# Performance work log

Measured on AMD Instinct MI355X. Metric: run time of the kernel, lower is better.

Reference implementation:

```python
import math
import jax, jax.numpy as jnp
import numpy as np

D_MODEL = 1024
NUM_HEADS = 16
HEAD_DIM = D_MODEL // NUM_HEADS
MAX_REL = 128


def setup_inputs() -> dict:
    key = jax.random.key(0)
    ks = jax.random.split(key, 7)
    B, S = 2, 2048
    s = 1.0 / math.sqrt(D_MODEL)
    return {
        "x": jax.random.normal(ks[0], (B, S, D_MODEL), dtype=jnp.float32),
        "mask": jnp.ones((B, S, S), dtype=jnp.int32),
        "w_q": jax.random.normal(ks[1], (D_MODEL, D_MODEL), dtype=jnp.float32) * s,
        "w_k": jax.random.normal(ks[2], (D_MODEL, D_MODEL), dtype=jnp.float32) * s,
        "w_v": jax.random.normal(ks[3], (D_MODEL, D_MODEL), dtype=jnp.float32) * s,
        "w_o_w": jax.random.normal(ks[4], (D_MODEL, D_MODEL), dtype=jnp.float32) * s,
        "w_o_b": jnp.zeros((D_MODEL,), dtype=jnp.float32),
        "rel_emb": jax.random.normal(ks[5], (2 * MAX_REL + 1, HEAD_DIM), dtype=jnp.float32),
    }


def reference(x, mask, w_q, w_k, w_v, w_o_w, w_o_b, rel_emb):
    B, S, D = x.shape
    H, hd = NUM_HEADS, HEAD_DIM
    scale = math.sqrt(hd)

    def proj(w):  # torch Linear: x @ w.T  -> [B,H,S,hd]
        return (x @ w.T).reshape(B, S, H, hd).transpose(0, 2, 1, 3)

    Q, K, V = proj(w_q), proj(w_k), proj(w_v)

    # content scores (scaled)
    scores = jnp.einsum("bhqd,bhkd->bhqk", Q, K) / scale

    # T5-style relative position bias (NOT scaled, matching source)
    pos = jnp.arange(S)
    dist = jnp.clip(pos[None, :] - pos[:, None], -MAX_REL, MAX_REL) + MAX_REL  # [S,S]
    rel = rel_emb[dist]  # [S,S,hd]
    scores = scores + jnp.einsum("bhqd,qkd->bhqk", Q, rel)

    scores = jnp.where(mask[:, None, :, :] == 0, -1e9, scores)
    attn = jax.nn.softmax(scores, axis=-1)  # [B,H,S,S]

    ctx = jnp.einsum("bhqk,bhkd->bhqd", attn, V)
    ctx = ctx.transpose(0, 2, 1, 3).reshape(B, S, D)
    out = ctx @ w_o_w.T + w_o_b
    return out, attn
```

## Files before the change

### kernel.cpp

```cpp
#include <hip/hip_runtime.h>
#include <hip/hip_bf16.h>

#define B_ 2
#define S_ 2048
#define H_ 16
#define HD_ 64
#define D_ 1024
#define NJ_ 257
#define RSTRIDE_ 264

typedef __bf16 v8bf __attribute__((ext_vector_type(8)));
typedef __bf16 v4bf __attribute__((ext_vector_type(4)));
typedef float  v4f  __attribute__((ext_vector_type(4)));

static __device__ __forceinline__ v4f mfma16(v8bf a, v8bf b, v4f c) {
    return __builtin_amdgcn_mfma_f32_16x16x32_bf16(a, b, c, 0, 0, 0);
}

__global__ void k_split2(const float* __restrict__ src, __bf16* __restrict__ h,
                         __bf16* __restrict__ l, int n4) {
    int i = blockIdx.x * blockDim.x + threadIdx.x;
    int stride = gridDim.x * blockDim.x;
    for (; i < n4; i += stride) {
        const float4 v = ((const float4*)src)[i];
        float vv[4] = {v.x, v.y, v.z, v.w};
        v4bf hv, lv;
#pragma unroll
        for (int j = 0; j < 4; j++) {
            __bf16 hb = (__bf16)vv[j];
            hv[j] = hb;
            lv[j] = (__bf16)(vv[j] - (float)hb);
        }
        *(v4bf*)(h + 4 * (size_t)i) = hv;
        *(v4bf*)(l + 4 * (size_t)i) = lv;
    }
}

__global__ void k_cast4(const float* __restrict__ w0, const float* __restrict__ w1,
                        const float* __restrict__ w2, const float* __restrict__ w3,
                        __bf16* __restrict__ o0, __bf16* __restrict__ o1,
                        __bf16* __restrict__ o2, __bf16* __restrict__ o3) {
    const int n4each = (D_ * D_) / 4;
    int i = blockIdx.x * blockDim.x + threadIdx.x;
    int stride = gridDim.x * blockDim.x;
    for (; i < 4 * n4each; i += stride) {
        const int region = i >> 18, j = i & (n4each - 1);
        const float* src = region == 0 ? w0 : region == 1 ? w1 : region == 2 ? w2 : w3;
        __bf16* dst = region == 0 ? o0 : region == 1 ? o1 : region == 2 ? o2 : o3;
        const float4 v = ((const float4*)src)[j];
        v4bf o = {(__bf16)v.x, (__bf16)v.y, (__bf16)v.z, (__bf16)v.w};
        *(v4bf*)(dst + 4 * (size_t)j) = o;
    }
}

__global__ void k_rowflag(const int* __restrict__ mask, unsigned char* __restrict__ flags) {
    const int row = blockIdx.x;
    const int4* mp = (const int4*)(mask + (size_t)row * S_);
    int ok = 1;
    for (int i = threadIdx.x; i < S_ / 4; i += blockDim.x) {
        int4 m = mp[i];
        ok &= (m.x != 0) & (m.y != 0) & (m.z != 0) & (m.w != 0);
    }
    int all = __syncthreads_and(ok);
    if (threadIdx.x == 0) flags[row] = (unsigned char)(all != 0);
}

__global__ __launch_bounds__(256) void k_projQKV(const __bf16* __restrict__ xh,
                                                 const __bf16* __restrict__ xl,
                                                 const __bf16* __restrict__ wqh,
                                                 const __bf16* __restrict__ wkh,
                                                 const __bf16* __restrict__ wvh,
                                                 __bf16* __restrict__ Qh,
                                                 __bf16* __restrict__ Ql,
                                                 __bf16* __restrict__ Kh,
                                                 __bf16* __restrict__ Vb) {
    __shared__ __bf16 sXh[64][72], sXl[64][72], sW[64][72];
    const int seg = blockIdx.x >> 4;
    const int n0 = (blockIdx.x & 15) * 64;
    const int m0 = blockIdx.y * 64;
    const __bf16* W = seg == 0 ? wqh : (seg == 1 ? wkh : wvh);
    const int tid = threadIdx.x, lane = tid & 63, wid = tid >> 6;
    const int fr = lane & 15, fo = (lane >> 4) * 8;
    const int srow = tid >> 2, scol = (tid & 3) * 16;
    v4f acc[4] = {};
    for (int k0 = 0; k0 < D_; k0 += 64) {
        const size_t ga = (size_t)(m0 + srow) * D_ + k0 + scol;
        const size_t gb = (size_t)(n0 + srow) * D_ + k0 + scol;
        *(v8bf*)&sXh[srow][scol]     = *(const v8bf*)(xh + ga);
        *(v8bf*)&sXh[srow][scol + 8] = *(const v8bf*)(xh + ga + 8);
        if (seg < 2) {
            *(v8bf*)&sXl[srow][scol]     = *(const v8bf*)(xl + ga);
            *(v8bf*)&sXl[srow][scol + 8] = *(const v8bf*)(xl + ga + 8);
        }
        *(v8bf*)&sW[srow][scol]     = *(const v8bf*)(W + gb);
        *(v8bf*)&sW[srow][scol + 8] = *(const v8bf*)(W + gb + 8);
        __syncthreads();
#pragma unroll
        for (int ks = 0; ks < 2; ks++) {
            v8bf ah = *(const v8bf*)&sXh[wid * 16 + fr][ks * 32 + fo];
            v8bf al;
            if (seg < 2) al = *(const v8bf*)&sXl[wid * 16 + fr][ks * 32 + fo];
#pragma unroll
            for (int nt = 0; nt < 4; nt++) {
                v8bf bb = *(const v8bf*)&sW[nt * 16 + fr][ks * 32 + fo];
                acc[nt] = mfma16(ah, bb, acc[nt]);
                if (seg < 2) acc[nt] = mfma16(al, bb, acc[nt]);
            }
        }
        __syncthreads();
    }
#pragma unroll
    for (int nt = 0; nt < 4; nt++) {
#pragma unroll
        for (int r = 0; r < 4; r++) {
            const int row = m0 + wid * 16 + (lane >> 4) * 4 + r;
            const int col = n0 + nt * 16 + fr;
            const size_t idx = (size_t)row * D_ + col;
            const float f = acc[nt][r];
            if (seg == 0) {
                __bf16 hb = (__bf16)f;
                Qh[idx] = hb;
                Ql[idx] = (__bf16)(f - (float)hb);
            } else if (seg == 1) {
                Kh[idx] = (__bf16)f;
            } else {
                Vb[idx] = (__bf16)f;
            }
        }
    }
}

__global__ __launch_bounds__(256) void k_vtrans(const __bf16* __restrict__ Vb,
                                                __bf16* __restrict__ Vt) {
    __shared__ __bf16 t[64][72];
    const int s0 = blockIdx.x * 64, n0 = blockIdx.y * 64, b = blockIdx.z;
    const int tid = threadIdx.x;
    const int r = tid >> 2, c = (tid & 3) * 16;
    const size_t gin = ((size_t)(b * S_ + s0 + r)) * D_ + n0 + c;
    *(v8bf*)&t[r][c]     = *(const v8bf*)(Vb + gin);
    *(v8bf*)&t[r][c + 8] = *(const v8bf*)(Vb + gin + 8);
    __syncthreads();
    v8bf o0, o1;
#pragma unroll
    for (int j = 0; j < 8; j++) { o0[j] = t[c + j][r]; o1[j] = t[c + 8 + j][r]; }
    const size_t gout = ((size_t)(b * D_ + n0 + r)) * S_ + s0 + c;
    *(v8bf*)(Vt + gout)     = o0;
    *(v8bf*)(Vt + gout + 8) = o1;
}

__global__ __launch_bounds__(256) void k_relgemm(const __bf16* __restrict__ Qh,
                                                 const __bf16* __restrict__ Ql,
                                                 const __bf16* __restrict__ relh,
                                                 const __bf16* __restrict__ rell,
                                                 float* __restrict__ Rg,
                                                 float* __restrict__ qnorm,
                                                 float* __restrict__ Rmax) {
    const int q0 = blockIdx.x * 64;
    const int bh = blockIdx.y;
    const int b = bh >> 4, h = bh & 15;
    const int tid = threadIdx.x, lane = tid & 63, wid = tid >> 6;
    const int fr = lane & 15, fo = (lane >> 4) * 8;
    const size_t qbase = (size_t)(b * S_ + q0 + wid * 16 + fr) * D_ + h * HD_;
    v8bf qa_h[2], qa_l[2];
#pragma unroll
    for (int ks = 0; ks < 2; ks++) {
        qa_h[ks] = *(const v8bf*)(Qh + qbase + ks * 32 + fo);
        qa_l[ks] = *(const v8bf*)(Ql + qbase + ks * 32 + fo);
    }

    float qs = 0.0f;
#pragma unroll
    for (int ks = 0; ks < 2; ks++)
#pragma unroll
        for (int j = 0; j < 8; j++) {
            const float v = (float)qa_h[ks][j] + (float)qa_l[ks][j];
            qs += v * v;
        }
    qs += __shfl_xor(qs, 16);
    qs += __shfl_xor(qs, 32);
    if ((lane >> 4) == 0) qnorm[(size_t)bh * S_ + q0 + wid * 16 + fr] = sqrtf(qs);

    v4f acc[17] = {};
#pragma unroll
    for (int jt = 0; jt < 17; jt++) {
        int j = jt * 16 + fr;
        if (j > 256) j = 256;
        const size_t rb = (size_t)j * HD_;
#pragma unroll
        for (int ks = 0; ks < 2; ks++) {
            v8bf bh_ = *(const v8bf*)(relh + rb + ks * 32 + fo);
            v8bf bl_ = *(const v8bf*)(rell + rb + ks * 32 + fo);
            acc[jt] = mfma16(qa_h[ks], bh_, acc[jt]);
            acc[jt] = mfma16(qa_h[ks], bl_, acc[jt]);
            acc[jt] = mfma16(qa_l[ks], bh_, acc[jt]);
        }
    }

    float rm[4] = {-3.0e38f, -3.0e38f, -3.0e38f, -3.0e38f};
#pragma unroll
    for (int jt = 0; jt < 17; jt++)
#pragma unroll
        for (int r = 0; r < 4; r++) rm[r] = fmaxf(rm[r], acc[jt][r]);
#pragma unroll
    for (int r = 0; r < 4; r++) {
#pragma unroll
        for (int sh = 1; sh < 16; sh <<= 1) rm[r] = fmaxf(rm[r], __shfl_xor(rm[r], sh));
    }
    if (fr == 0) {
#pragma unroll
        for (int r = 0; r < 4; r++)
            Rmax[(size_t)bh * S_ + q0 + wid * 16 + (lane >> 4) * 4 + r] = rm[r];
    }

    const size_t rowbase = ((size_t)bh * S_ + q0 + wid * 16 + (lane >> 4) * 4) * RSTRIDE_;
#pragma unroll
    for (int jt = 0; jt < 17; jt++) {
        const int j = jt * 16 + fr;
        if (j <= 256) {
#pragma unroll
            for (int r = 0; r < 4; r++)
                Rg[rowbase + (size_t)r * RSTRIDE_ + j] = acc[jt][r];
        }
    }
}

__global__ __launch_bounds__(256) void k_knorm(const __bf16* __restrict__ Kh,
                                               float* __restrict__ Kmax) {
    __shared__ float red[4];
    const int bh = blockIdx.x, b = bh >> 4, h = bh & 15;
    const int tid = threadIdx.x;
    float best = 0.0f;
#pragma unroll
    for (int i = 0; i < 8; i++) {
        const int k = tid + i * 256;
        const __bf16* kr = Kh + (size_t)(b * S_ + k) * D_ + h * HD_;
        float s = 0.0f;
#pragma unroll
        for (int j = 0; j < 8; j++) {
            v8bf v = *(const v8bf*)(kr + j * 8);
#pragma unroll
            for (int e = 0; e < 8; e++) { const float f = (float)v[e]; s += f * f; }
        }
        best = fmaxf(best, s);
    }
#pragma unroll
    for (int sh = 1; sh < 64; sh <<= 1) best = fmaxf(best, __shfl_xor(best, sh));
    if ((tid & 63) == 0) red[tid >> 6] = best;
    __syncthreads();
    if (tid == 0)
        Kmax[bh] = sqrtf(fmaxf(fmaxf(red[0], red[1]), fmaxf(red[2], red[3])));
}

__global__ __launch_bounds__(512, 4) void k_attnE(const __bf16* __restrict__ Qh,
                                                  const __bf16* __restrict__ Ql,
                                                  const __bf16* __restrict__ Kh,
                                                  const __bf16* __restrict__ Vt,
                                                  const float* __restrict__ Rg,
                                                  const int* __restrict__ mask,
                                                  const unsigned char* __restrict__ flags,
                                                  const float* __restrict__ qnorm,
                                                  const float* __restrict__ Rmax,
                                                  const float* __restrict__ Kmax,
                                                  __bf16* __restrict__ E,
                                                  float* __restrict__ lrowInv,
                                                  __bf16* __restrict__ ctx) {
    __shared__ __bf16 sK[2][64][72], sV[2][64][72], sP[128][72];
    const int flat = blockIdx.x;
    const int swz = (flat & 7) * 64 + (flat >> 3);
    const int qt = swz & 15, bh = swz >> 4;
    const int b = bh >> 4, h = bh & 15;
    const int q0 = qt * 128;
    const int tid = threadIdx.x, lane = tid & 63, w = tid >> 6;
    const int fr = lane & 15, fq = lane >> 4, fo = fq * 8;
    const int myrow = w * 16 + fq * 4;
    const int srow = tid >> 3, sc8 = (tid & 7) * 8;

    const size_t qbase = (size_t)(b * S_ + q0 + w * 16 + fr) * D_ + h * HD_;
    v8bf qa_h[2], qa_l[2];
#pragma unroll
    for (int ks = 0; ks < 2; ks++) {
        qa_h[ks] = *(const v8bf*)(Qh + qbase + ks * 32 + fo);
        qa_l[ks] = *(const v8bf*)(Ql + qbase + ks * 32 + fo);
    }

    const int qg0 = q0 + myrow;
    const size_t rbase0 = ((size_t)bh * S_ + qg0) * RSTRIDE_;
    const size_t mbase0 = ((size_t)b * S_ + qg0) * S_;
    float rcL[4], rcR[4], mhat[4];
    int flr[4];
    const float km = Kmax[bh] * 0.125f;
#pragma unroll
    for (int r = 0; r < 4; r++) {
        rcL[r] = Rg[rbase0 + (size_t)r * RSTRIDE_];
        rcR[r] = Rg[rbase0 + (size_t)r * RSTRIDE_ + 256];
        flr[r] = flags[(size_t)b * S_ + qg0 + r];
        mhat[r] = Rmax[(size_t)bh * S_ + qg0 + r] +
                  qnorm[(size_t)bh * S_ + qg0 + r] * km + 0.5f;
    }

    const __bf16* kgbase = Kh + (size_t)(b * S_ + srow) * D_ + h * HD_ + sc8;
    const __bf16* vgbase = Vt + (size_t)(b * D_ + h * HD_ + srow) * S_ + sc8;
    v8bf rk = *(const v8bf*)(kgbase);
    v8bf rv = *(const v8bf*)(vgbase);
    *(v8bf*)&sK[0][srow][sc8] = rk;
    *(v8bf*)&sV[0][srow][sc8] = rv;
    rk = *(const v8bf*)(kgbase + (size_t)64 * D_);
    rv = *(const v8bf*)(vgbase + 64);
    __syncthreads();

    float lrun[4] = {0.0f, 0.0f, 0.0f, 0.0f};
    v4f acc2[4] = {};
    int cur = 0;
    for (int kc = 0; kc < 32; kc++) {
        const int k0 = kc * 64;
        v4f acc[4] = {};
#pragma unroll
        for (int ct = 0; ct < 4; ct++) {
#pragma unroll
            for (int ks = 0; ks < 2; ks++) {
                v8bf kb = *(const v8bf*)&sK[cur][ct * 16 + fr][ks * 32 + fo];
                acc[ct] = mfma16(qa_h[ks], kb, acc[ct]);
                acc[ct] = mfma16(qa_l[ks], kb, acc[ct]);
            }
        }
        const bool band = (kc >= 2 * qt - 3) && (kc <= 2 * qt + 3);
        const bool left = kc < 2 * qt;
#pragma unroll
        for (int r = 0; r < 4; r++) {
            const int qg = qg0 + r;
#pragma unroll
            for (int ct = 0; ct < 4; ct++) {
                const int k = k0 + ct * 16 + fr;
                float bias;
                if (band) {
                    const int dd = k - qg;
                    const int j = dd < -128 ? 0 : (dd > 128 ? 256 : dd + 128);
                    bias = Rg[rbase0 + (size_t)r * RSTRIDE_ + j];
                } else {
                    bias = left ? rcL[r] : rcR[r];
                }
                float sv = acc[ct][r] * 0.125f + bias;
                if (!flr[r] && mask[mbase0 + (size_t)r * S_ + k] == 0) sv = -1e9f;
                const float e = __expf(sv - mhat[r]);
                lrun[r] += e;
                sP[myrow + r][ct * 16 + fr] = (__bf16)e;
            }
        }
        __syncthreads();

#pragma unroll
        for (int ks = 0; ks < 2; ks++) {
            v8bf pa = *(const v8bf*)&sP[w * 16 + fr][ks * 32 + fo];
#pragma unroll
            for (int ct = 0; ct < 4; ct++) {
                v8bf vb = *(const v8bf*)&sV[cur][ct * 16 + fr][ks * 32 + fo];
                acc2[ct] = mfma16(pa, vb, acc2[ct]);
            }
        }
#pragma unroll
        for (int i = 0; i < 2; i++) {
            const int rl = (tid >> 3) + i * 64;
            *(v8bf*)(E + ((size_t)bh * S_ + q0 + rl) * S_ + k0 + sc8) =
                *(const v8bf*)&sP[rl][sc8];
        }
        if (kc < 31) {
            *(v8bf*)&sK[cur ^ 1][srow][sc8] = rk;
            *(v8bf*)&sV[cur ^ 1][srow][sc8] = rv;
        }
        if (kc < 30) {
            rk = *(const v8bf*)(kgbase + (size_t)(k0 + 128) * D_);
            rv = *(const v8bf*)(vgbase + k0 + 128);
        }
        __syncthreads();
        cur ^= 1;
    }

    float invl[4];
#pragma unroll
    for (int r = 0; r < 4; r++) {
#pragma unroll
        for (int sh = 1; sh < 16; sh <<= 1) lrun[r] += __shfl_xor(lrun[r], sh);
        invl[r] = 1.0f / (lrun[r] + 1e-37f);
    }
    if (fr == 0) {
#pragma unroll
        for (int r = 0; r < 4; r++) lrowInv[(size_t)bh * S_ + qg0 + r] = invl[r];
    }

#pragma unroll
    for (int ct = 0; ct < 4; ct++) {
#pragma unroll
        for (int r = 0; r < 4; r++) {
            const int qg = qg0 + r;
            const int d = ct * 16 + fr;
            ctx[(size_t)(b * S_ + qg) * D_ + h * HD_ + d] = (__bf16)(acc2[ct][r] * invl[r]);
        }
    }
}

__global__ __launch_bounds__(256) void k_rescale(const __bf16* __restrict__ E,
                                                 const float* __restrict__ lrowInv,
                                                 float* __restrict__ attn) {
    const size_t total8 = (size_t)B_ * H_ * S_ * S_ / 8;
    size_t i = (size_t)blockIdx.x * blockDim.x + threadIdx.x;
    const size_t stride = (size_t)gridDim.x * blockDim.x;
    for (; i < total8; i += stride) {
        const float inv = lrowInv[i >> 8];
        const v8bf e = *(const v8bf*)(E + i * 8);
        float4 o0, o1;
        o0.x = (float)e[0] * inv; o0.y = (float)e[1] * inv;
        o0.z = (float)e[2] * inv; o0.w = (float)e[3] * inv;
        o1.x = (float)e[4] * inv; o1.y = (float)e[5] * inv;
        o1.z = (float)e[6] * inv; o1.w = (float)e[7] * inv;
        *(float4*)(attn + i * 8)     = o0;
        *(float4*)(attn + i * 8 + 4) = o1;
    }
}

__global__ __launch_bounds__(256) void k_outproj(const __bf16* __restrict__ A,
                                                 const __bf16* __restrict__ Bw,
                                                 const float* __restrict__ bias,
                                                 float* __restrict__ out) {
    __shared__ __bf16 sA[64][72], sB[64][72];
    const int n0 = blockIdx.x * 64;
    const int m0 = blockIdx.y * 64;
    const int tid = threadIdx.x, lane = tid & 63, wid = tid >> 6;
    const int fr = lane & 15, fo = (lane >> 4) * 8;
    const int srow = tid >> 2, scol = (tid & 3) * 16;
    v4f acc[4] = {};
    for (int k0 = 0; k0 < D_; k0 += 64) {
        const size_t ga = (size_t)(m0 + srow) * D_ + k0 + scol;
        const size_t gb = (size_t)(n0 + srow) * D_ + k0 + scol;
        *(v8bf*)&sA[srow][scol]     = *(const v8bf*)(A + ga);
        *(v8bf*)&sA[srow][scol + 8] = *(const v8bf*)(A + ga + 8);
        *(v8bf*)&sB[srow][scol]     = *(const v8bf*)(Bw + gb);
        *(v8bf*)&sB[srow][scol + 8] = *(const v8bf*)(Bw + gb + 8);
        __syncthreads();
#pragma unroll
        for (int ks = 0; ks < 2; ks++) {
            v8bf a = *(const v8bf*)&sA[wid * 16 + fr][ks * 32 + fo];
#pragma unroll
            for (int nt = 0; nt < 4; nt++) {
                v8bf bb = *(const v8bf*)&sB[nt * 16 + fr][ks * 32 + fo];
                acc[nt] = mfma16(a, bb, acc[nt]);
            }
        }
        __syncthreads();
    }
#pragma unroll
    for (int nt = 0; nt < 4; nt++) {
        const float bv = bias[n0 + nt * 16 + fr];
#pragma unroll
        for (int r = 0; r < 4; r++) {
            const int row = m0 + wid * 16 + (lane >> 4) * 4 + r;
            out[(size_t)row * D_ + n0 + nt * 16 + fr] = acc[nt][r] + bv;
        }
    }
}

extern "C" void kernel_launch(void* const* d_in, const int* in_sizes, int n_in,
                              void* d_out, int out_size, void* d_ws, size_t ws_size,
                              hipStream_t stream) {
    (void)in_sizes; (void)n_in; (void)out_size; (void)ws_size;
    const float* x    = (const float*)d_in[0];
    const int*   mask = (const int*)d_in[1];
    const float* wq   = (const float*)d_in[2];
    const float* wk   = (const float*)d_in[3];
    const float* wv   = (const float*)d_in[4];
    const float* wo   = (const float*)d_in[5];
    const float* wob  = (const float*)d_in[6];
    const float* rel  = (const float*)d_in[7];
    float* out  = (float*)d_out;
    float* attn = out + (size_t)B_ * S_ * D_;

    char* p = (char*)d_ws;
    auto alloc = [&](size_t bytes) -> char* {
        char* r = p;
        p += (bytes + 255) & ~(size_t)255;
        return r;
    };
    const size_t BSD = (size_t)B_ * S_ * D_;
    const size_t DD  = (size_t)D_ * D_;
    const size_t BHS = (size_t)B_ * H_ * S_;
    __bf16* xh   = (__bf16*)alloc(BSD * 2);
    __bf16* xl   = (__bf16*)alloc(BSD * 2);
    __bf16* wqh  = (__bf16*)alloc(DD * 2);
    __bf16* wkh  = (__bf16*)alloc(DD * 2);
    __bf16* wvh  = (__bf16*)alloc(DD * 2);
    __bf16* woh  = (__bf16*)alloc(DD * 2);
    __bf16* relh = (__bf16*)alloc((size_t)NJ_ * HD_ * 2);
    __bf16* rell = (__bf16*)alloc((size_t)NJ_ * HD_ * 2);
    __bf16* Qh   = (__bf16*)alloc(BSD * 2);
    __bf16* Ql   = (__bf16*)alloc(BSD * 2);
    __bf16* Kh   = (__bf16*)alloc(BSD * 2);
    __bf16* Vb   = (__bf16*)alloc(BSD * 2);
    __bf16* Vt   = (__bf16*)alloc(BSD * 2);
    float*  Rg   = (float*)alloc(BHS * RSTRIDE_ * 4);
    float*  qn   = (float*)alloc(BHS * 4);
    float*  Rmax = (float*)alloc(BHS * 4);
    float*  Kmax = (float*)alloc((size_t)B_ * H_ * 4);
    float*  lrowInv = (float*)alloc(BHS * 4);
    __bf16* E    = (__bf16*)alloc((size_t)B_ * H_ * S_ * S_ * 2);
    __bf16* ctx  = (__bf16*)alloc(BSD * 2);
    unsigned char* flags = (unsigned char*)alloc((size_t)B_ * S_);

    k_split2<<<2048, 256, 0, stream>>>(x, xh, xl, (int)(BSD / 4));
    k_split2<<<17, 256, 0, stream>>>(rel, relh, rell, (int)(NJ_ * HD_ / 4));
    k_cast4<<<1024, 256, 0, stream>>>(wq, wk, wv, wo, wqh, wkh, wvh, woh);

    k_rowflag<<<B_ * S_, 256, 0, stream>>>(mask, flags);

    k_projQKV<<<dim3(48, B_ * S_ / 64), 256, 0, stream>>>(xh, xl, wqh, wkh, wvh,
                                                          Qh, Ql, Kh, Vb);

    k_vtrans<<<dim3(S_ / 64, D_ / 64, B_), 256, 0, stream>>>(Vb, Vt);

    k_relgemm<<<dim3(S_ / 64, B_ * H_), 256, 0, stream>>>(Qh, Ql, relh, rell, Rg, qn, Rmax);

    k_knorm<<<B_ * H_, 256, 0, stream>>>(Kh, Kmax);

    k_attnE<<<512, 512, 0, stream>>>(Qh, Ql, Kh, Vt, Rg, mask, flags, qn, Rmax, Kmax,
                                     E, lrowInv, ctx);

    k_rescale<<<4096, 256, 0, stream>>>(E, lrowInv, attn);

    k_outproj<<<dim3(D_ / 64, B_ * S_ / 64), 256, 0, stream>>>(ctx, woh, wob, out);
}
```

Baseline: 581.5 us.

## Fuse attention-probability rescale into attention kernel and drop block barrier

The separate rescale kernel is removed. Each attention block now keeps its row inverse-normalisers in shared memory and, after the main loop, reads back its own unnormalised bf16 tile of E and writes the normalised fp32 attention probabilities. The E store is remapped so that each wave copies only the sP rows it wrote itself, which lets the barrier between writing sP and the PV MFMA be dropped. This saves a kernel launch and the lrowInv round trip, and the E reread is likely to hit in cache. In exchange the attention kernel gets a long store-heavy tail, and the code now relies on wave-synchronous shared-memory visibility.

```diff
diff --git a/kernel.cpp b/kernel.cpp
--- a/kernel.cpp
+++ b/kernel.cpp
@@ -262,9 +262,10 @@
                                                   const float* __restrict__ Rmax,
                                                   const float* __restrict__ Kmax,
                                                   __bf16* __restrict__ E,
-                                                  float* __restrict__ lrowInv,
+                                                  float* __restrict__ attn,
                                                   __bf16* __restrict__ ctx) {
     __shared__ __bf16 sK[2][64][72], sV[2][64][72], sP[128][72];
+    __shared__ float sLi[128];
     const int flat = blockIdx.x;
     const int swz = (flat & 7) * 64 + (flat >> 3);
     const int qt = swz & 15, bh = swz >> 4;
@@ -297,6 +298,10 @@
         mhat[r] = Rmax[(size_t)bh * S_ + qg0 + r] +
                   qnorm[(size_t)bh * S_ + qg0 + r] * km + 0.5f;
     }
+
+    const int erow = w * 16 + (lane >> 2);
+    const int ecol = (lane & 3) * 16;
+    __bf16* ebase = E + ((size_t)bh * S_ + q0 + erow) * S_ + ecol;
 
     const __bf16* kgbase = Kh + (size_t)(b * S_ + srow) * D_ + h * HD_ + sc8;
     const __bf16* vgbase = Vt + (size_t)(b * D_ + h * HD_ + srow) * S_ + sc8;
@@ -346,8 +351,6 @@
                 sP[myrow + r][ct * 16 + fr] = (__bf16)e;
             }
         }
-        __syncthreads();
-
 #pragma unroll
         for (int ks = 0; ks < 2; ks++) {
             v8bf pa = *(const v8bf*)&sP[w * 16 + fr][ks * 32 + fo];
@@ -357,12 +360,8 @@
                 acc2[ct] = mfma16(pa, vb, acc2[ct]);
             }
         }
-#pragma unroll
-        for (int i = 0; i < 2; i++) {
-            const int rl = (tid >> 3) + i * 64;
-            *(v8bf*)(E + ((size_t)bh * S_ + q0 + rl) * S_ + k0 + sc8) =
-                *(const v8bf*)&sP[rl][sc8];
-        }
+        *(v8bf*)(ebase + k0)     = *(const v8bf*)&sP[erow][ecol];
+        *(v8bf*)(ebase + k0 + 8) = *(const v8bf*)&sP[erow][ecol + 8];
         if (kc < 31) {
             *(v8bf*)&sK[cur ^ 1][srow][sc8] = rk;
             *(v8bf*)&sV[cur ^ 1][srow][sc8] = rv;
@@ -384,7 +383,7 @@
     }
     if (fr == 0) {
 #pragma unroll
-        for (int r = 0; r < 4; r++) lrowInv[(size_t)bh * S_ + qg0 + r] = invl[r];
+        for (int r = 0; r < 4; r++) sLi[myrow + r] = invl[r];
     }
 
 #pragma unroll
@@ -396,24 +395,25 @@
             ctx[(size_t)(b * S_ + qg) * D_ + h * HD_ + d] = (__bf16)(acc2[ct][r] * invl[r]);
         }
     }
-}
-
-__global__ __launch_bounds__(256) void k_rescale(const __bf16* __restrict__ E,
-                                                 const float* __restrict__ lrowInv,
-                                                 float* __restrict__ attn) {
-    const size_t total8 = (size_t)B_ * H_ * S_ * S_ / 8;
-    size_t i = (size_t)blockIdx.x * blockDim.x + threadIdx.x;
-    const size_t stride = (size_t)gridDim.x * blockDim.x;
-    for (; i < total8; i += stride) {
-        const float inv = lrowInv[i >> 8];
-        const v8bf e = *(const v8bf*)(E + i * 8);
+
+    __syncthreads();
+
+    const __bf16* Eblk = E + ((size_t)bh * S_ + q0) * S_;
+    float* ablk = attn + ((size_t)bh * S_ + q0) * S_;
+#pragma unroll 4
+    for (int it = 0; it < 64; it++) {
+        const int g = tid + it * 512;
+        const int row = g >> 8;
+        const int col8 = (g & 255) * 8;
+        const float inv = sLi[row];
+        const v8bf e = *(const v8bf*)(Eblk + (size_t)row * S_ + col8);
         float4 o0, o1;
         o0.x = (float)e[0] * inv; o0.y = (float)e[1] * inv;
         o0.z = (float)e[2] * inv; o0.w = (float)e[3] * inv;
         o1.x = (float)e[4] * inv; o1.y = (float)e[5] * inv;
         o1.z = (float)e[6] * inv; o1.w = (float)e[7] * inv;
-        *(float4*)(attn + i * 8)     = o0;
-        *(float4*)(attn + i * 8 + 4) = o1;
+        *(float4*)(ablk + (size_t)row * S_ + col8)     = o0;
+        *(float4*)(ablk + (size_t)row * S_ + col8 + 4) = o1;
     }
 }
 
@@ -499,7 +499,6 @@
     float*  qn   = (float*)alloc(BHS * 4);
     float*  Rmax = (float*)alloc(BHS * 4);
     float*  Kmax = (float*)alloc((size_t)B_ * H_ * 4);
-    float*  lrowInv = (float*)alloc(BHS * 4);
     __bf16* E    = (__bf16*)alloc((size_t)B_ * H_ * S_ * S_ * 2);
     __bf16* ctx  = (__bf16*)alloc(BSD * 2);
     unsigned char* flags = (unsigned char*)alloc((size_t)B_ * S_);
@@ -520,9 +519,7 @@
     k_knorm<<<B_ * H_, 256, 0, stream>>>(Kh, Kmax);
 
     k_attnE<<<512, 512, 0, stream>>>(Qh, Ql, Kh, Vt, Rg, mask, flags, qn, Rmax, Kmax,
-                                     E, lrowInv, ctx);
-
-    k_rescale<<<4096, 256, 0, stream>>>(E, lrowInv, attn);
+                                     E, attn, ctx);
 
     k_outproj<<<dim3(D_ / 64, B_ * S_ / 64), 256, 0, stream>>>(ctx, woh, wob, out);
 }
```

Result: faster. 560.1 us (-3.7%).
